# Kernel tuning notes

Hardware: AMD Instinct MI355X
Metric: run time of the kernel (lower is better)

The kernel has to match this reference:

```python
import jax, jax.numpy as jnp
import numpy as np

B_SZ, SEQ, D_MODEL = 2, 4096, 2048
D_INNER, D_STATE, D_XB, D_CONV = 2048, 128, 512, 4
NHEADS = D_INNER // D_STATE      # 16 heads
HEADDIM = D_STATE                # 128 (module sets headdim = d_state)
NKV = D_XB // HEADDIM            # 4 kv heads
N_REP = D_INNER // D_XB          # 4 (num_kv_groups)
CHUNK = 256
CONV_DIM = D_INNER + 2 * D_XB    # 3072
D_IN_PROJ = D_INNER + 2 * D_XB + D_INNER + NHEADS  # z | x,B,C | dt


def setup_inputs() -> dict:
    key = jax.random.key(0)
    ks = jax.random.split(key, 8)
    # dt_bias init per module: inverse-softplus of dt ~ logU(1e-3, 0.1)
    dt = jnp.exp(jax.random.uniform(ks[4], (NHEADS,)) * (np.log(0.1) - np.log(0.001)) + np.log(0.001))
    dt_bias = dt + jnp.log(-jnp.expm1(-dt))
    A_log = jnp.log(jax.random.uniform(ks[5], (NHEADS,), minval=1.0, maxval=16.0))
    return {
        "hidden_states": jax.random.normal(ks[0], (B_SZ, SEQ, D_MODEL), jnp.float32),
        "in_proj_w": jax.random.normal(ks[1], (D_IN_PROJ, D_MODEL), jnp.float32) * 0.02,
        "conv_w": jax.random.normal(ks[2], (CONV_DIM, D_CONV), jnp.float32) * 0.2,
        "conv_b": jnp.zeros((CONV_DIM,), jnp.float32),
        "dt_bias": dt_bias.astype(jnp.float32),
        "A_log": A_log.astype(jnp.float32),
        "D": jnp.ones((NHEADS,), jnp.float32),
        "norm_w": jnp.ones((D_INNER,), jnp.float32),
        "out_proj_w": jax.random.normal(ks[3], (D_MODEL, D_INNER), jnp.float32) * 0.02,
    }


def _ssd(x, dt, A, Bm, Cm):
    """Chunked Mamba2 SSD scan. x:[b,l,h,p] dt:[b,l,h] A:[h] Bm:[b,l,h,n] Cm:[b,l,h,n]."""
    b, l, h, p = x.shape
    c = l // CHUNK
    resh = lambda t: t.reshape(b, c, CHUNK, *t.shape[2:])
    x, dt, Bm, Cm = resh(x), resh(dt), resh(Bm), resh(Cm)
    xdt = x * dt[..., None]                       # [b,c,cl,h,p]
    dA = (dt * A).transpose(0, 3, 1, 2)           # [b,h,c,cl]
    Acs = jnp.cumsum(dA, axis=-1)                 # [b,h,c,cl]
    # intra-chunk causal decay matrix L (segment-sum), masked before exp for safe grads
    seg = Acs[..., :, None] - Acs[..., None, :]   # [b,h,c,cl,cl]
    mask = jnp.tril(jnp.ones((CHUNK, CHUNK), bool))
    Lmat = jnp.where(mask, jnp.exp(jnp.where(mask, seg, 0.0)), 0.0)
    Y_diag = jnp.einsum('bclhn,bcshn,bhcls,bcshp->bclhp', Cm, Bm, Lmat, xdt)
    # per-chunk end states
    decay_states = jnp.exp(Acs[..., -1:] - Acs)   # [b,h,c,cl]
    states = jnp.einsum('bclhn,bhcl,bclhp->bchpn', Bm, decay_states, xdt)
    chunk_decay = jnp.exp(Acs[..., -1])           # [b,h,c]
    # inter-chunk recurrence (scan over c chunks)
    states_t = jnp.swapaxes(states, 0, 1)         # [c,b,h,p,n]
    decay_t = jnp.transpose(chunk_decay, (2, 0, 1))  # [c,b,h]

    def step(carry, inputs):
        s, d = inputs
        return carry * d[..., None, None] + s, carry

    _, prev = jax.lax.scan(step, jnp.zeros_like(states_t[0]), (states_t, decay_t))
    prev = jnp.swapaxes(prev, 0, 1)               # [b,c,h,p,n] state entering each chunk
    Y_off = jnp.einsum('bclhn,bchpn,bhcl->bclhp', Cm, prev, jnp.exp(Acs))
    return (Y_diag + Y_off).reshape(b, l, h, p)


def reference(hidden_states, in_proj_w, conv_w, conv_b, dt_bias, A_log, D, norm_w, out_proj_w):
    b, l, _ = hidden_states.shape
    zxbcdt = hidden_states @ in_proj_w.T          # [b,l,5136]
    z = zxbcdt[..., :D_INNER]
    xBC = zxbcdt[..., D_INNER:D_INNER + CONV_DIM]
    dt = zxbcdt[..., D_INNER + CONV_DIM:]         # [b,l,H]
    # causal depthwise conv1d (pad left d_conv-1, take first L) + SiLU
    xp = jnp.pad(xBC, ((0, 0), (D_CONV - 1, 0), (0, 0)))
    conv = conv_b + sum(xp[:, k:k + l, :] * conv_w[:, k] for k in range(D_CONV))
    xBC = jax.nn.silu(conv)
    x = xBC[..., :D_XB].reshape(b, l, NKV, HEADDIM)
    Bm = xBC[..., D_XB:2 * D_XB].reshape(b, l, NKV, HEADDIM)
    Cm = xBC[..., 2 * D_XB:].reshape(b, l, NHEADS, D_STATE)
    x = jnp.repeat(x, N_REP, axis=2)              # repeat_kv (GQA)
    Bm = jnp.repeat(Bm, N_REP, axis=2)
    dt = jax.nn.softplus(dt + dt_bias)
    A = -jnp.exp(A_log)
    y = _ssd(x, dt, A, Bm, Cm) + D[None, None, :, None] * x  # [b,l,h,p]
    # gated per-head RMSNorm (norm_before_gate=False, group_size=headdim)
    g = y.reshape(b, l, D_INNER) * jax.nn.silu(z)
    gr = g.reshape(b, l, NHEADS, HEADDIM)
    rstd = jax.lax.rsqrt(jnp.mean(gr * gr, axis=-1, keepdims=True) + 1e-5)
    yn = (gr * rstd).reshape(b, l, D_INNER) * norm_w
    return yn @ out_proj_w.T
```

## Files before the change

### kernel.cpp

```cpp
#include <hip/hip_runtime.h>

typedef unsigned short u16t;
typedef __attribute__((ext_vector_type(8))) short bf8;
typedef __attribute__((ext_vector_type(4))) float f4;

#define DEV __device__ __forceinline__

DEV u16t f2b(float f){
  unsigned u = __float_as_uint(f);
  u = (u + 0x7fffu + ((u >> 16) & 1u)) >> 16;
  return (u16t)u;
}
DEV float b2f(u16t u){ return __uint_as_float(((unsigned)u) << 16); }
DEV float sigm(float x){ return 1.f / (1.f + __expf(-x)); }

typedef __attribute__((address_space(1))) const void gas1;
typedef __attribute__((address_space(3))) void las3;
DEV void gl_lds16(const void* g, void* l){
  __builtin_amdgcn_global_load_lds((gas1*)g, (las3*)l, 16, 0, 0);
}

constexpr int KDIM   = 2048;
constexpr int DPROJ  = 5136;
constexpr int BLROWS = 8192;
constexpr int NT32   = KDIM / 32;

#define MFMA16(a,b,c) __builtin_amdgcn_mfma_f32_16x16x32_bf16((a),(b),(c),0,0,0)

__global__ __launch_bounds__(256) void k_cvt(const float* __restrict__ src,
                                             u16t* __restrict__ dst, int n4){
  int i = blockIdx.x * 256 + threadIdx.x;
  if (i < n4){
    float4 v = ((const float4*)src)[i];
    ushort4 o;
    o.x = f2b(v.x); o.y = f2b(v.y); o.z = f2b(v.z); o.w = f2b(v.w);
    ((ushort4*)dst)[i] = o;
  }
}

template<bool NCLAMP>
DEV void gemm128(const u16t* __restrict__ Ag, const u16t* __restrict__ Wg,
                 char* lds, int m0, int n0, f4 (&acc)[4][4]){
  const int tid = threadIdx.x;
  const int lane = tid & 63, w = tid >> 6;
  const int lo = lane & 15, hi = lane >> 4;
  const int wm = w >> 2, wn = w & 3;
  const int srow = tid >> 2;
  const int scol = ((tid & 3) ^ ((tid >> 3) & 3)) << 3;
  const int sdst = w << 10;
#pragma unroll
  for (int i = 0; i < 4; ++i)
#pragma unroll
    for (int j = 0; j < 4; ++j) acc[i][j] = (f4){0.f, 0.f, 0.f, 0.f};

  auto STAGE_A = [&](int d, int t){
    gl_lds16(Ag + (size_t)(m0 + srow) * KDIM + (t << 5) + scol,
             lds + d * 24576 + sdst);
  };
  auto STAGE_B = [&](int d, int op, int t){
    int r = n0 + op * 128 + srow;
    if (NCLAMP && r > DPROJ - 1) r = DPROJ - 1;
    gl_lds16(Wg + (size_t)r * KDIM + (t << 5) + scol,
             lds + d * 24576 + 8192 + op * 8192 + sdst);
  };
  auto RD_A = [&](const char* Ab, bf8 (&afr)[4]){
#pragma unroll
    for (int f = 0; f < 4; ++f){
      int row = wm * 64 + f * 16 + lo;
      afr[f] = *(const bf8*)(Ab + ((row >> 1) << 7) + ((row & 1) << 6)
                                + (((hi ^ (row >> 1)) & 3) << 4));
    }
  };
  auto RD_B = [&](const char* Bb, bf8 (&bfr)[4]){
#pragma unroll
    for (int f = 0; f < 4; ++f){
      int row = wn * 64 + f * 16 + lo;
      bfr[f] = *(const bf8*)(Bb + ((row >> 1) << 7) + ((row & 1) << 6)
                                + (((hi ^ (row >> 1)) & 3) << 4));
    }
  };

  STAGE_A(0, 0); STAGE_B(0, 0, 0); STAGE_B(0, 1, 0);
  asm volatile("s_waitcnt vmcnt(0)" ::: "memory");
  __builtin_amdgcn_s_barrier();

  for (int t = 0; t < NT32; ++t){
    const int d = t & 1, dn = d ^ 1;
    const char* Ab = lds + d * 24576;
    const char* Bb = Ab + 8192;
    bf8 afr[4], bfr[4];
    RD_B(Bb, bfr); RD_A(Ab, afr);
    if (t + 1 < NT32){ STAGE_A(dn, t + 1); STAGE_B(dn, 0, t + 1); STAGE_B(dn, 1, t + 1); }
    __builtin_amdgcn_s_setprio(1);
#pragma unroll
    for (int f = 0; f < 4; ++f)
#pragma unroll
      for (int n = 0; n < 4; ++n)
        acc[f][n] = MFMA16(afr[f], bfr[n], acc[f][n]);
    __builtin_amdgcn_s_setprio(0);
    asm volatile("s_waitcnt vmcnt(0)" ::: "memory");
    __builtin_amdgcn_s_barrier();
  }
}

__global__ __launch_bounds__(512, 2) void k_gemm_in(const u16t* __restrict__ Ag,
                                                    const u16t* __restrict__ Wg,
                                                    u16t* __restrict__ z16,
                                                    u16t* __restrict__ xbc16,
                                                    float* __restrict__ dtraw){
  __shared__ __align__(16) char lds[49152];
  int id = blockIdx.x;
  int orig = (id & 7) * 168 + (id >> 3);
  int bx = orig % 21, by = orig / 21;
  const int m0 = by << 7, n0 = bx << 8;
  f4 acc[4][4];
  gemm128<true>(Ag, Wg, lds, m0, n0, acc);
  const int tid = threadIdx.x;
  const int lane = tid & 63, w = tid >> 6;
  const int lo = lane & 15, hi = lane >> 4;
  const int wm = w >> 2, wn = w & 3;
#pragma unroll
  for (int fm = 0; fm < 4; ++fm)
#pragma unroll
    for (int fn = 0; fn < 4; ++fn){
      int col = n0 + wn * 64 + fn * 16 + lo;
#pragma unroll
      for (int i = 0; i < 4; ++i){
        int r = m0 + wm * 64 + fm * 16 + hi * 4 + i;
        float v = acc[fm][fn][i];
        if (col < 2048)       z16[(size_t)r * 2048 + col] = f2b(v);
        else if (col < 5120)  xbc16[(size_t)r * 3072 + (col - 2048)] = f2b(v);
        else if (col < 5136)  dtraw[(size_t)r * 16 + (col - 5120)] = v;
      }
    }
}

__global__ __launch_bounds__(512, 2) void k_gemm_out(const u16t* __restrict__ Ag,
                                                     const u16t* __restrict__ Wg,
                                                     float* __restrict__ C){
  __shared__ __align__(16) char lds[49152];
  int id = blockIdx.x;
  int orig = (id & 7) * 64 + (id >> 3);
  int bx = orig % 8, by = orig / 8;
  const int m0 = by << 7, n0 = bx << 8;
  f4 acc[4][4];
  gemm128<false>(Ag, Wg, lds, m0, n0, acc);
  const int tid = threadIdx.x;
  const int lane = tid & 63, w = tid >> 6;
  const int lo = lane & 15, hi = lane >> 4;
  const int wm = w >> 2, wn = w & 3;
#pragma unroll
  for (int fm = 0; fm < 4; ++fm)
#pragma unroll
    for (int fn = 0; fn < 4; ++fn){
      int col = n0 + wn * 64 + fn * 16 + lo;
#pragma unroll
      for (int i = 0; i < 4; ++i){
        int r = m0 + wm * 64 + fm * 16 + hi * 4 + i;
        C[(size_t)r * 2048 + col] = acc[fm][fn][i];
      }
    }
}

__global__ __launch_bounds__(256) void k_conv(const u16t* __restrict__ xbc,
                                              const float* __restrict__ cw,
                                              const float* __restrict__ cb,
                                              u16t* __restrict__ xf16,
                                              u16t* __restrict__ Bg,
                                              u16t* __restrict__ Cgb){
  int ch = blockIdx.x * 1024 + threadIdx.x * 4;
  int b  = blockIdx.z;
  int l0 = blockIdx.y * 64;
  float4 cbv = *(const float4*)(cb + ch);
  float4 w0 = *(const float4*)(cw + ch * 4);
  float4 w1 = *(const float4*)(cw + ch * 4 + 4);
  float4 w2 = *(const float4*)(cw + ch * 4 + 8);
  float4 w3 = *(const float4*)(cw + ch * 4 + 12);
  const u16t* rowp = xbc + ((size_t)(b * 4096 + l0)) * 3072 + ch;
  float4 p3 = {0.f,0.f,0.f,0.f}, p2 = p3, p1 = p3;
  if (l0 > 0){
    ushort4 v;
    v = *(const ushort4*)(rowp - 3 * 3072); p3 = {b2f(v.x), b2f(v.y), b2f(v.z), b2f(v.w)};
    v = *(const ushort4*)(rowp - 2 * 3072); p2 = {b2f(v.x), b2f(v.y), b2f(v.z), b2f(v.w)};
    v = *(const ushort4*)(rowp - 1 * 3072); p1 = {b2f(v.x), b2f(v.y), b2f(v.z), b2f(v.w)};
  }
  for (int i = 0; i < 64; ++i){
    ushort4 v = *(const ushort4*)rowp;
    float4 cur = {b2f(v.x), b2f(v.y), b2f(v.z), b2f(v.w)};
    float a0 = cbv.x + p3.x * w0.x + p2.x * w0.y + p1.x * w0.z + cur.x * w0.w;
    float a1 = cbv.y + p3.y * w1.x + p2.y * w1.y + p1.y * w1.z + cur.y * w1.w;
    float a2 = cbv.z + p3.z * w2.x + p2.z * w2.y + p1.z * w2.z + cur.z * w2.w;
    float a3 = cbv.w + p3.w * w3.x + p2.w * w3.y + p1.w * w3.z + cur.w * w3.w;
    ushort4 o;
    o.x = f2b(a0 * sigm(a0)); o.y = f2b(a1 * sigm(a1));
    o.z = f2b(a2 * sigm(a2)); o.w = f2b(a3 * sigm(a3));
    size_t bl = (size_t)b * 4096 + l0 + i;
    if (ch < 512)       *(ushort4*)(xf16 + bl * 512 + ch) = o;
    else if (ch < 1024) *(ushort4*)(Bg + bl * 512 + (ch - 512)) = o;
    else                *(ushort4*)(Cgb + bl * 2048 + (ch - 1024)) = o;
    p3 = p2; p2 = p1; p1 = cur;
    rowp += 3072;
  }
}

__global__ __launch_bounds__(256) void k_dt(const float* __restrict__ dtraw,
                                            const float* __restrict__ dtb,
                                            float* __restrict__ dtv){
  int bl = blockIdx.x * 256 + threadIdx.x;
  int b = bl >> 12, l = bl & 4095;
#pragma unroll
  for (int h = 0; h < 16; ++h){
    float x = dtraw[(size_t)bl * 16 + h] + dtb[h];
    float sp = (x > 15.f) ? x : log1pf(__expf(x));
    dtv[((size_t)(b * 16 + h)) * 4096 + l] = sp;
  }
}

__global__ __launch_bounds__(256) void k_prep(const float* __restrict__ dtv,
                                              const float* __restrict__ alog,
                                              float* __restrict__ Acs,
                                              float* __restrict__ dstv,
                                              float* __restrict__ cdec){
  int c = blockIdx.x, h = blockIdx.y, b = blockIdx.z;
  int tid = threadIdx.x;
  int bhc = (b * 16 + h) * 16 + c;
  __shared__ float sb_[2][256];
  float An = -__expf(alog[h]);
  float dA = dtv[((size_t)(b * 16 + h)) * 4096 + c * 256 + tid] * An;
  sb_[0][tid] = dA;
  __syncthreads();
  int src = 0;
  for (int off = 1; off < 256; off <<= 1){
    float v = sb_[src][tid];
    if (tid >= off) v += sb_[src][tid - off];
    sb_[src ^ 1][tid] = v;
    __syncthreads();
    src ^= 1;
  }
  float a = sb_[src][tid];
  float ae = sb_[src][255];
  Acs[(size_t)bhc * 256 + tid]  = a;
  dstv[(size_t)bhc * 256 + tid] = __expf(ae - a);
  if (tid == 0) cdec[bhc] = __expf(ae);
}

__global__ __launch_bounds__(256) void k_repack(const u16t* __restrict__ xf16,
                                                const float* __restrict__ dtv,
                                                const u16t* __restrict__ Bg,
                                                u16t* __restrict__ xdtT,
                                                u16t* __restrict__ BgT){
  int c = blockIdx.x, h = blockIdx.y, b = blockIdx.z;
  int tid = threadIdx.x;
  int bhc = (b * 16 + h) * 16 + c;
  int kv = h >> 2;
  __shared__ float tile[128][65];
  for (int st = 0; st < 4; ++st){
#pragma unroll
    for (int i = 0; i < 32; ++i){
      int idx = i * 256 + tid;
      int sl = idx >> 7, p = idx & 127;
      int l = c * 256 + st * 64 + sl;
      size_t bl = (size_t)b * 4096 + l;
      tile[p][sl] = b2f(xf16[bl * 512 + kv * 128 + p]) * dtv[((size_t)(b * 16 + h)) * 4096 + l];
    }
    __syncthreads();
#pragma unroll
    for (int i = 0; i < 32; ++i){
      int idx = i * 256 + tid;
      int p = idx >> 6, sl = idx & 63;
      xdtT[(size_t)bhc * 32768 + p * 256 + st * 64 + sl] = f2b(tile[p][sl]);
    }
    __syncthreads();
  }
  if (h < 4){
    for (int st = 0; st < 4; ++st){
#pragma unroll
      for (int i = 0; i < 32; ++i){
        int idx = i * 256 + tid;
        int sl = idx >> 7, n = idx & 127;
        size_t bl = (size_t)b * 4096 + c * 256 + st * 64 + sl;
        tile[n][sl] = (float)Bg[bl * 512 + h * 128 + n];
      }
      __syncthreads();
#pragma unroll
      for (int i = 0; i < 32; ++i){
        int idx = i * 256 + tid;
        int n = idx >> 6, sl = idx & 63;
        BgT[((size_t)(b * 4 + h) * 128 + n) * 4096 + c * 256 + st * 64 + sl] = (u16t)tile[n][sl];
      }
      __syncthreads();
    }
  }
}

__global__ __launch_bounds__(256) void k_states(const u16t* __restrict__ xdtT,
                                                const float* __restrict__ dstv,
                                                const u16t* __restrict__ BgT,
                                                u16t* __restrict__ states16){
  int c = blockIdx.x, h = blockIdx.y, b = blockIdx.z;
  int tid = threadIdx.x, lane = tid & 63, w = tid >> 6;
  int lo = lane & 15, hi = lane >> 4;
  int bhc = (b * 16 + h) * 16 + c;
  int kv = h >> 2;
  f4 zero = {0.f, 0.f, 0.f, 0.f};
  f4 acc[2][8];
#pragma unroll
  for (int i = 0; i < 2; ++i)
#pragma unroll
    for (int j = 0; j < 8; ++j) acc[i][j] = zero;
#pragma unroll
  for (int kk = 0; kk < 8; ++kk){
    f4 d0 = *(const f4*)(dstv + (size_t)bhc * 256 + kk * 32 + hi * 8);
    f4 d1 = *(const f4*)(dstv + (size_t)bhc * 256 + kk * 32 + hi * 8 + 4);
    bf8 af[2];
#pragma unroll
    for (int pr = 0; pr < 2; ++pr){
      bf8 a = *(const bf8*)(xdtT + (size_t)bhc * 32768 + (w * 32 + pr * 16 + lo) * 256 + kk * 32 + hi * 8);
      bf8 ad;
#pragma unroll
      for (int j = 0; j < 4; ++j){
        ad[j]     = (short)f2b(b2f((u16t)a[j]) * d0[j]);
        ad[4 + j] = (short)f2b(b2f((u16t)a[4 + j]) * d1[j]);
      }
      af[pr] = ad;
    }
    bf8 bb[8];
#pragma unroll
    for (int nb = 0; nb < 8; ++nb)
      bb[nb] = *(const bf8*)(BgT + ((size_t)(b * 4 + kv) * 128 + nb * 16 + lo) * 4096 + c * 256 + kk * 32 + hi * 8);
#pragma unroll
    for (int pr = 0; pr < 2; ++pr)
#pragma unroll
      for (int nb = 0; nb < 8; ++nb)
        acc[pr][nb] = MFMA16(af[pr], bb[nb], acc[pr][nb]);
  }
#pragma unroll
  for (int pr = 0; pr < 2; ++pr)
#pragma unroll
    for (int nb = 0; nb < 8; ++nb)
#pragma unroll
      for (int i = 0; i < 4; ++i)
        states16[(size_t)bhc * 16384 + (w * 32 + pr * 16 + hi * 4 + i) * 128 + nb * 16 + lo]
          = f2b(acc[pr][nb][i]);
}

__global__ __launch_bounds__(256) void k_scan(const u16t* __restrict__ states16,
                                              const float* __restrict__ cdec,
                                              u16t* __restrict__ prevb){
  int h = blockIdx.x, b = blockIdx.y, sl = blockIdx.z;
  int tid = threadIdx.x;
  int bh = b * 16 + h;
  float carry[8];
#pragma unroll
  for (int i = 0; i < 8; ++i) carry[i] = 0.f;
  for (int c = 0; c < 16; ++c){
    size_t base = ((size_t)bh * 16 + c) * 16384 + sl * 2048;
    float cd = cdec[bh * 16 + c];
#pragma unroll
    for (int i = 0; i < 8; ++i){
      size_t idx = base + i * 256 + tid;
      prevb[idx] = f2b(carry[i]);
      carry[i] = carry[i] * cd + b2f(states16[idx]);
    }
  }
}

__global__ __launch_bounds__(256) void k_fin(const u16t* __restrict__ Cg,
                                             const u16t* __restrict__ Bg,
                                             const u16t* __restrict__ xdtT,
                                             const u16t* __restrict__ prevb,
                                             const float* __restrict__ Acs,
                                             const u16t* __restrict__ z16,
                                             const u16t* __restrict__ xf16,
                                             const float* __restrict__ Dp,
                                             const float* __restrict__ nw,
                                             u16t* __restrict__ yn){
  int c = blockIdx.x, h = blockIdx.y, b = blockIdx.z;
  int tid = threadIdx.x, lane = tid & 63, w = tid >> 6;
  int lo = lane & 15, hi = lane >> 4;
  int bhc = (b * 16 + h) * 16 + c;
  int kv = h >> 2;
  int blbase = b * 4096 + c * 256;
  __shared__ float AcsS[256];
  __shared__ __align__(16) char Gb[4][8192];
  AcsS[tid] = Acs[(size_t)bhc * 256 + tid];
  __syncthreads();
  char* gw = Gb[w];
  f4 zero = {0.f, 0.f, 0.f, 0.f};
  f4 accY[4][8];
#pragma unroll
  for (int i = 0; i < 4; ++i)
#pragma unroll
    for (int j = 0; j < 8; ++j) accY[i][j] = zero;
  float eav[4];
#pragma unroll
  for (int mb = 0; mb < 4; ++mb)
    eav[mb] = __expf(AcsS[w * 64 + mb * 16 + lo]);
#pragma unroll
  for (int kk = 0; kk < 4; ++kk){
    bf8 af[4], bb[8];
#pragma unroll
    for (int mb = 0; mb < 4; ++mb){
      int l = w * 64 + mb * 16 + lo;
      bf8 cr = *(const bf8*)(Cg + (size_t)(blbase + l) * 2048 + h * 128 + kk * 32 + hi * 8);
      bf8 cs;
#pragma unroll
      for (int j = 0; j < 8; ++j) cs[j] = (short)f2b(b2f((u16t)cr[j]) * eav[mb]);
      af[mb] = cs;
    }
#pragma unroll
    for (int pb = 0; pb < 8; ++pb)
      bb[pb] = *(const bf8*)(prevb + (size_t)bhc * 16384 + (pb * 16 + lo) * 128 + kk * 32 + hi * 8);
#pragma unroll
    for (int mb = 0; mb < 4; ++mb)
#pragma unroll
      for (int pb = 0; pb < 8; ++pb)
        accY[mb][pb] = MFMA16(af[mb], bb[pb], accY[mb][pb]);
  }
  for (int sb = 0; sb <= w; ++sb){
    f4 g[4][4];
#pragma unroll
    for (int i = 0; i < 4; ++i)
#pragma unroll
      for (int j = 0; j < 4; ++j) g[i][j] = zero;
#pragma unroll
    for (int kk = 0; kk < 4; ++kk){
      bf8 af[4], bb[4];
#pragma unroll
      for (int mb = 0; mb < 4; ++mb)
        af[mb] = *(const bf8*)(Cg + (size_t)(blbase + w * 64 + mb * 16 + lo) * 2048 + h * 128 + kk * 32 + hi * 8);
#pragma unroll
      for (int nb = 0; nb < 4; ++nb)
        bb[nb] = *(const bf8*)(Bg + (size_t)(blbase + sb * 64 + nb * 16 + lo) * 512 + kv * 128 + kk * 32 + hi * 8);
#pragma unroll
      for (int mb = 0; mb < 4; ++mb)
#pragma unroll
        for (int nb = 0; nb < 4; ++nb)
          g[mb][nb] = MFMA16(af[mb], bb[nb], g[mb][nb]);
    }
#pragma unroll
    for (int mb = 0; mb < 4; ++mb)
#pragma unroll
      for (int nb = 0; nb < 4; ++nb)
#pragma unroll
        for (int i = 0; i < 4; ++i){
          int lrow = w * 64 + mb * 16 + hi * 4 + i;
          int scol = sb * 64 + nb * 16 + lo;
          float v = g[mb][nb][i];
          v = (scol <= lrow) ? v * __expf(AcsS[lrow] - AcsS[scol]) : 0.f;
          int rl = mb * 16 + hi * 4 + i;
          int off = ((rl << 7) + ((nb * 16 + lo) << 1)) ^ ((rl & 7) << 4);
          *(u16t*)(gw + off) = f2b(v);
        }
#pragma unroll
    for (int k2 = 0; k2 < 2; ++k2){
      bf8 a2[4], b2[8];
#pragma unroll
      for (int mb = 0; mb < 4; ++mb){
        int rl = mb * 16 + lo;
        int off = ((rl << 7) + (k2 << 6) + (hi << 4)) ^ ((rl & 7) << 4);
        a2[mb] = *(const bf8*)(gw + off);
      }
#pragma unroll
      for (int pb = 0; pb < 8; ++pb)
        b2[pb] = *(const bf8*)(xdtT + (size_t)bhc * 32768 + (pb * 16 + lo) * 256 + sb * 64 + k2 * 32 + hi * 8);
#pragma unroll
      for (int mb = 0; mb < 4; ++mb)
#pragma unroll
        for (int pb = 0; pb < 8; ++pb)
          accY[mb][pb] = MFMA16(a2[mb], b2[pb], accY[mb][pb]);
    }
  }
  float Dh = Dp[h];
#pragma unroll
  for (int mb = 0; mb < 4; ++mb){
#pragma unroll
    for (int i = 0; i < 4; ++i){
      int lrow = w * 64 + mb * 16 + hi * 4 + i;
      size_t bl = (size_t)blbase + lrow;
      float gv[8];
      float ss = 0.f;
#pragma unroll
      for (int pb = 0; pb < 8; ++pb){
        int p = pb * 16 + lo;
        float y = accY[mb][pb][i] + Dh * b2f(xf16[bl * 512 + kv * 128 + p]);
        float z = b2f(z16[bl * 2048 + h * 128 + p]);
        float g = y * z * sigm(z);
        gv[pb] = g;
        ss += g * g;
      }
      ss += __shfl_xor(ss, 1);
      ss += __shfl_xor(ss, 2);
      ss += __shfl_xor(ss, 4);
      ss += __shfl_xor(ss, 8);
      float rstd = rsqrtf(ss * (1.f / 128.f) + 1e-5f);
#pragma unroll
      for (int pb = 0; pb < 8; ++pb){
        int p = pb * 16 + lo;
        yn[bl * 2048 + h * 128 + p] = f2b(gv[pb] * rstd * nw[h * 128 + p]);
      }
    }
  }
}

extern "C" void kernel_launch(void* const* d_in, const int* in_sizes, int n_in,
                              void* d_out, int out_size, void* d_ws, size_t ws_size,
                              hipStream_t stream){
  const float* hs   = (const float*)d_in[0];
  const float* ipw  = (const float*)d_in[1];
  const float* cw   = (const float*)d_in[2];
  const float* cb   = (const float*)d_in[3];
  const float* dtb  = (const float*)d_in[4];
  const float* alog = (const float*)d_in[5];
  const float* Dp   = (const float*)d_in[6];
  const float* nw   = (const float*)d_in[7];
  const float* opw  = (const float*)d_in[8];
  float* out = (float*)d_out;

  char* base = (char*)d_ws;
  size_t o = 0;
  auto take = [&](size_t n) -> size_t { size_t r = o; o += (n + 255) & ~(size_t)255; return r; };

  size_t offA = take(33554432);
  u16t* X16      = (u16t*)(base + offA);
  u16t* states16 = (u16t*)(base + offA);
  u16t* prevb    = (u16t*)(base + offA + 16777216);
  size_t offB = take(21037056);
  u16t*  Wp16 = (u16t*)(base + offB);
  u16t*  BgT  = (u16t*)(base + offB);
  float* dtv  = (float*)(base + offB + 8388608);
  float* Acs  = (float*)(base + offB + 8912896);
  float* dstv = (float*)(base + offB + 9437184);
  float* cdec = (float*)(base + offB + 9961472);
  u16t*  Wo16 = (u16t*)(base + take(8388608));
  u16t*  z16  = (u16t*)(base + take(33554432));
  size_t offC = take(50331648);
  u16t* xbc16 = (u16t*)(base + offC);
  u16t* yn16  = (u16t*)(base + offC);
  float* dtraw = (float*)(base + take(524288));
  u16t*  xf16  = (u16t*)(base + take(8388608));
  u16t*  Bg    = (u16t*)(base + take(8388608));
  u16t*  Cgb   = (u16t*)(base + take(33554432));
  u16t*  xdtT  = (u16t*)(base + take(33554432));

  if (ws_size < o) return;

  k_cvt<<<16384, 256, 0, stream>>>(hs, X16, BLROWS * 2048 / 4);
  k_cvt<<<10272, 256, 0, stream>>>(ipw, Wp16, DPROJ * 2048 / 4);
  k_cvt<<<4096, 256, 0, stream>>>(opw, Wo16, 2048 * 2048 / 4);
  k_gemm_in<<<1344, 512, 0, stream>>>(X16, Wp16, z16, xbc16, dtraw);
  k_conv<<<dim3(3, 64, 2), 256, 0, stream>>>(xbc16, cw, cb, xf16, Bg, Cgb);
  k_dt<<<32, 256, 0, stream>>>(dtraw, dtb, dtv);
  k_prep<<<dim3(16, 16, 2), 256, 0, stream>>>(dtv, alog, Acs, dstv, cdec);
  k_repack<<<dim3(16, 16, 2), 256, 0, stream>>>(xf16, dtv, Bg, xdtT, BgT);
  k_states<<<dim3(16, 16, 2), 256, 0, stream>>>(xdtT, dstv, BgT, states16);
  k_scan<<<dim3(16, 2, 8), 256, 0, stream>>>(states16, cdec, prevb);
  k_fin<<<dim3(16, 16, 2), 256, 0, stream>>>(Cgb, Bg, xdtT, prevb, Acs, z16, xf16, Dp, nw, yn16);
  k_gemm_out<<<512, 512, 0, stream>>>(yn16, Wo16, out);
}
```

Baseline: 630.8 us.

## Split k_fin per chunk-half, fuse dt softplus into prep, widen scan grid

Removes the k_dt kernel by computing softplus of dt inside k_prep, which now also writes dtv, saving a launch and a round trip of dt. k_scan is split across twice as many blocks, each carrying four state rows instead of eight. k_fin now launches two blocks per chunk, each handling 128 rows with 32 rows per wave and 32-column causal sub-blocks, with a smaller LDS tile under a new swizzle. The aim is more blocks and better balance of the triangular work on the many CUs, at the cost of loading prevb and B/C tiles again per half-block.

```diff
diff --git a/kernel.cpp b/kernel.cpp
--- a/kernel.cpp
+++ b/kernel.cpp
@@ -203,21 +203,10 @@
   }
 }
 
-__global__ __launch_bounds__(256) void k_dt(const float* __restrict__ dtraw,
-                                            const float* __restrict__ dtb,
-                                            float* __restrict__ dtv){
-  int bl = blockIdx.x * 256 + threadIdx.x;
-  int b = bl >> 12, l = bl & 4095;
-#pragma unroll
-  for (int h = 0; h < 16; ++h){
-    float x = dtraw[(size_t)bl * 16 + h] + dtb[h];
-    float sp = (x > 15.f) ? x : log1pf(__expf(x));
-    dtv[((size_t)(b * 16 + h)) * 4096 + l] = sp;
-  }
-}
-
-__global__ __launch_bounds__(256) void k_prep(const float* __restrict__ dtv,
+__global__ __launch_bounds__(256) void k_prep(const float* __restrict__ dtraw,
+                                              const float* __restrict__ dtb,
                                               const float* __restrict__ alog,
+                                              float* __restrict__ dtv,
                                               float* __restrict__ Acs,
                                               float* __restrict__ dstv,
                                               float* __restrict__ cdec){
@@ -225,9 +214,12 @@
   int tid = threadIdx.x;
   int bhc = (b * 16 + h) * 16 + c;
   __shared__ float sb_[2][256];
+  size_t bl = (size_t)b * 4096 + c * 256 + tid;
+  float x = dtraw[bl * 16 + h] + dtb[h];
+  float sp = (x > 15.f) ? x : log1pf(__expf(x));
+  dtv[((size_t)(b * 16 + h)) * 4096 + c * 256 + tid] = sp;
   float An = -__expf(alog[h]);
-  float dA = dtv[((size_t)(b * 16 + h)) * 4096 + c * 256 + tid] * An;
-  sb_[0][tid] = dA;
+  sb_[0][tid] = sp * An;
   __syncthreads();
   int src = 0;
   for (int off = 1; off < 256; off <<= 1){
@@ -350,14 +342,14 @@
   int h = blockIdx.x, b = blockIdx.y, sl = blockIdx.z;
   int tid = threadIdx.x;
   int bh = b * 16 + h;
-  float carry[8];
-#pragma unroll
-  for (int i = 0; i < 8; ++i) carry[i] = 0.f;
+  float carry[4];
+#pragma unroll
+  for (int i = 0; i < 4; ++i) carry[i] = 0.f;
   for (int c = 0; c < 16; ++c){
-    size_t base = ((size_t)bh * 16 + c) * 16384 + sl * 2048;
+    size_t base = ((size_t)bh * 16 + c) * 16384 + sl * 1024;
     float cd = cdec[bh * 16 + c];
 #pragma unroll
-    for (int i = 0; i < 8; ++i){
+    for (int i = 0; i < 4; ++i){
       size_t idx = base + i * 256 + tid;
       prevb[idx] = f2b(carry[i]);
       carry[i] = carry[i] * cd + b2f(states16[idx]);
@@ -375,33 +367,35 @@
                                              const float* __restrict__ Dp,
                                              const float* __restrict__ nw,
                                              u16t* __restrict__ yn){
-  int c = blockIdx.x, h = blockIdx.y, b = blockIdx.z;
+  int c2 = blockIdx.x, h = blockIdx.y, b = blockIdx.z;
+  int c = c2 >> 1, half = c2 & 1;
   int tid = threadIdx.x, lane = tid & 63, w = tid >> 6;
   int lo = lane & 15, hi = lane >> 4;
   int bhc = (b * 16 + h) * 16 + c;
   int kv = h >> 2;
   int blbase = b * 4096 + c * 256;
+  const int lbase = half * 128 + w * 32;
+  const int jmax = half * 4 + w;
   __shared__ float AcsS[256];
-  __shared__ __align__(16) char Gb[4][8192];
+  __shared__ __align__(16) char Gb[4][2048];
   AcsS[tid] = Acs[(size_t)bhc * 256 + tid];
   __syncthreads();
   char* gw = Gb[w];
-  f4 zero = {0.f, 0.f, 0.f, 0.f};
-  f4 accY[4][8];
-#pragma unroll
-  for (int i = 0; i < 4; ++i)
-#pragma unroll
-    for (int j = 0; j < 8; ++j) accY[i][j] = zero;
-  float eav[4];
-#pragma unroll
-  for (int mb = 0; mb < 4; ++mb)
-    eav[mb] = __expf(AcsS[w * 64 + mb * 16 + lo]);
+  f4 accY[2][8];
+#pragma unroll
+  for (int i = 0; i < 2; ++i)
+#pragma unroll
+    for (int j = 0; j < 8; ++j) accY[i][j] = (f4){0.f, 0.f, 0.f, 0.f};
+  float eav[2];
+#pragma unroll
+  for (int mb = 0; mb < 2; ++mb)
+    eav[mb] = __expf(AcsS[lbase + mb * 16 + lo]);
 #pragma unroll
   for (int kk = 0; kk < 4; ++kk){
-    bf8 af[4], bb[8];
-#pragma unroll
-    for (int mb = 0; mb < 4; ++mb){
-      int l = w * 64 + mb * 16 + lo;
+    bf8 af[2], bb[8];
+#pragma unroll
+    for (int mb = 0; mb < 2; ++mb){
+      int l = lbase + mb * 16 + lo;
       bf8 cr = *(const bf8*)(Cg + (size_t)(blbase + l) * 2048 + h * 128 + kk * 32 + hi * 8);
       bf8 cs;
 #pragma unroll
@@ -412,71 +406,70 @@
     for (int pb = 0; pb < 8; ++pb)
       bb[pb] = *(const bf8*)(prevb + (size_t)bhc * 16384 + (pb * 16 + lo) * 128 + kk * 32 + hi * 8);
 #pragma unroll
-    for (int mb = 0; mb < 4; ++mb)
+    for (int mb = 0; mb < 2; ++mb)
 #pragma unroll
       for (int pb = 0; pb < 8; ++pb)
         accY[mb][pb] = MFMA16(af[mb], bb[pb], accY[mb][pb]);
   }
-  for (int sb = 0; sb <= w; ++sb){
-    f4 g[4][4];
-#pragma unroll
-    for (int i = 0; i < 4; ++i)
-#pragma unroll
-      for (int j = 0; j < 4; ++j) g[i][j] = zero;
+  for (int sb = 0; sb <= jmax; ++sb){
+    f4 g[2][2];
+#pragma unroll
+    for (int i = 0; i < 2; ++i)
+#pragma unroll
+      for (int j = 0; j < 2; ++j) g[i][j] = (f4){0.f, 0.f, 0.f, 0.f};
 #pragma unroll
     for (int kk = 0; kk < 4; ++kk){
-      bf8 af[4], bb[4];
-#pragma unroll
-      for (int mb = 0; mb < 4; ++mb)
-        af[mb] = *(const bf8*)(Cg + (size_t)(blbase + w * 64 + mb * 16 + lo) * 2048 + h * 128 + kk * 32 + hi * 8);
-#pragma unroll
-      for (int nb = 0; nb < 4; ++nb)
-        bb[nb] = *(const bf8*)(Bg + (size_t)(blbase + sb * 64 + nb * 16 + lo) * 512 + kv * 128 + kk * 32 + hi * 8);
-#pragma unroll
-      for (int mb = 0; mb < 4; ++mb)
-#pragma unroll
-        for (int nb = 0; nb < 4; ++nb)
+      bf8 af[2], bb[2];
+#pragma unroll
+      for (int mb = 0; mb < 2; ++mb)
+        af[mb] = *(const bf8*)(Cg + (size_t)(blbase + lbase + mb * 16 + lo) * 2048 + h * 128 + kk * 32 + hi * 8);
+#pragma unroll
+      for (int nb = 0; nb < 2; ++nb)
+        bb[nb] = *(const bf8*)(Bg + (size_t)(blbase + sb * 32 + nb * 16 + lo) * 512 + kv * 128 + kk * 32 + hi * 8);
+#pragma unroll
+      for (int mb = 0; mb < 2; ++mb)
+#pragma unroll
+        for (int nb = 0; nb < 2; ++nb)
           g[mb][nb] = MFMA16(af[mb], bb[nb], g[mb][nb]);
     }
 #pragma unroll
-    for (int mb = 0; mb < 4; ++mb)
-#pragma unroll
-      for (int nb = 0; nb < 4; ++nb)
+    for (int mb = 0; mb < 2; ++mb)
+#pragma unroll
+      for (int nb = 0; nb < 2; ++nb)
 #pragma unroll
         for (int i = 0; i < 4; ++i){
-          int lrow = w * 64 + mb * 16 + hi * 4 + i;
-          int scol = sb * 64 + nb * 16 + lo;
+          int lrow = lbase + mb * 16 + hi * 4 + i;
+          int scol = sb * 32 + nb * 16 + lo;
           float v = g[mb][nb][i];
           v = (scol <= lrow) ? v * __expf(AcsS[lrow] - AcsS[scol]) : 0.f;
           int rl = mb * 16 + hi * 4 + i;
-          int off = ((rl << 7) + ((nb * 16 + lo) << 1)) ^ ((rl & 7) << 4);
+          int col = nb * 16 + lo;
+          int off = ((rl >> 1) << 7) + ((rl & 1) << 6)
+                  + ((col << 1) ^ (((rl >> 1) & 3) << 4));
           *(u16t*)(gw + off) = f2b(v);
         }
-#pragma unroll
-    for (int k2 = 0; k2 < 2; ++k2){
-      bf8 a2[4], b2[8];
-#pragma unroll
-      for (int mb = 0; mb < 4; ++mb){
-        int rl = mb * 16 + lo;
-        int off = ((rl << 7) + (k2 << 6) + (hi << 4)) ^ ((rl & 7) << 4);
-        a2[mb] = *(const bf8*)(gw + off);
-      }
+    bf8 a2[2], b2[8];
+#pragma unroll
+    for (int mb = 0; mb < 2; ++mb){
+      int rl = mb * 16 + lo;
+      a2[mb] = *(const bf8*)(gw + ((rl >> 1) << 7) + ((rl & 1) << 6)
+                                + ((hi << 4) ^ (((rl >> 1) & 3) << 4)));
+    }
+#pragma unroll
+    for (int pb = 0; pb < 8; ++pb)
+      b2[pb] = *(const bf8*)(xdtT + (size_t)bhc * 32768 + (pb * 16 + lo) * 256 + sb * 32 + hi * 8);
+#pragma unroll
+    for (int mb = 0; mb < 2; ++mb)
 #pragma unroll
       for (int pb = 0; pb < 8; ++pb)
-        b2[pb] = *(const bf8*)(xdtT + (size_t)bhc * 32768 + (pb * 16 + lo) * 256 + sb * 64 + k2 * 32 + hi * 8);
-#pragma unroll
-      for (int mb = 0; mb < 4; ++mb)
-#pragma unroll
-        for (int pb = 0; pb < 8; ++pb)
-          accY[mb][pb] = MFMA16(a2[mb], b2[pb], accY[mb][pb]);
-    }
+        accY[mb][pb] = MFMA16(a2[mb], b2[pb], accY[mb][pb]);
   }
   float Dh = Dp[h];
 #pragma unroll
-  for (int mb = 0; mb < 4; ++mb){
+  for (int mb = 0; mb < 2; ++mb){
 #pragma unroll
     for (int i = 0; i < 4; ++i){
-      int lrow = w * 64 + mb * 16 + hi * 4 + i;
+      int lrow = lbase + mb * 16 + hi * 4 + i;
       size_t bl = (size_t)blbase + lrow;
       float gv[8];
       float ss = 0.f;
@@ -550,11 +543,10 @@
   k_cvt<<<4096, 256, 0, stream>>>(opw, Wo16, 2048 * 2048 / 4);
   k_gemm_in<<<1344, 512, 0, stream>>>(X16, Wp16, z16, xbc16, dtraw);
   k_conv<<<dim3(3, 64, 2), 256, 0, stream>>>(xbc16, cw, cb, xf16, Bg, Cgb);
-  k_dt<<<32, 256, 0, stream>>>(dtraw, dtb, dtv);
-  k_prep<<<dim3(16, 16, 2), 256, 0, stream>>>(dtv, alog, Acs, dstv, cdec);
+  k_prep<<<dim3(16, 16, 2), 256, 0, stream>>>(dtraw, dtb, alog, dtv, Acs, dstv, cdec);
   k_repack<<<dim3(16, 16, 2), 256, 0, stream>>>(xf16, dtv, Bg, xdtT, BgT);
   k_states<<<dim3(16, 16, 2), 256, 0, stream>>>(xdtT, dstv, BgT, states16);
-  k_scan<<<dim3(16, 2, 8), 256, 0, stream>>>(states16, cdec, prevb);
-  k_fin<<<dim3(16, 16, 2), 256, 0, stream>>>(Cgb, Bg, xdtT, prevb, Acs, z16, xf16, Dp, nw, yn16);
+  k_scan<<<dim3(16, 2, 16), 256, 0, stream>>>(states16, cdec, prevb);
+  k_fin<<<dim3(32, 16, 2), 256, 0, stream>>>(Cgb, Bg, xdtT, prevb, Acs, z16, xf16, Dp, nw, yn16);
   k_gemm_out<<<512, 512, 0, stream>>>(yn16, Wo16, out);
 }
```

New measurement: 537.5 us. -14.8%, faster.
